# Kernel optimization log

Measured on AMD Instinct MI355X. Metric: run time of the kernel, lower is better.

Reference implementation:

```python
import jax, jax.numpy as jnp
import numpy as np

D, H, F, N, V, B, S, T = 512, 8, 2048, 2, 32000, 2, 1024, 1024


def _pe(seq_len, d):
    pos = np.arange(seq_len)[:, None].astype(np.float32)
    div = np.exp(np.arange(0, d, 2).astype(np.float32) * (-np.log(10000.0) / d))
    pe = np.zeros((seq_len, d), np.float32)
    pe[:, 0::2] = np.sin(pos * div)
    pe[:, 1::2] = np.cos(pos * div)
    return jnp.asarray(pe)


def _ln(x, g, b, eps=1e-6):
    # torch .var() default is unbiased (ddof=1)
    m = x.mean(-1, keepdims=True)
    v = jnp.sum((x - m) ** 2, -1, keepdims=True) / (x.shape[-1] - 1)
    return g * (x - m) / jnp.sqrt(v + eps) + b


def _mha(q, k, v, mask, w, b):
    # w: [4, D, D] (q,k,v,o); b: [4, D]
    Bq, Sq, Dm = q.shape
    Sk = k.shape[1]
    dk = Dm // H
    Q = (q @ w[0] + b[0]).reshape(Bq, Sq, H, dk).transpose(0, 2, 1, 3)
    K = (k @ w[1] + b[1]).reshape(Bq, Sk, H, dk).transpose(0, 2, 1, 3)
    Vv = (v @ w[2] + b[2]).reshape(Bq, Sk, H, dk).transpose(0, 2, 1, 3)
    s = jnp.einsum('bhqd,bhkd->bhqk', Q, K) / jnp.sqrt(jnp.float32(dk))
    s = jnp.where(mask == 0, jnp.float32(-1e9), s)
    a = jax.nn.softmax(s, axis=-1)
    o = jnp.einsum('bhqk,bhkd->bhqd', a, Vv).transpose(0, 2, 1, 3).reshape(Bq, Sq, Dm)
    return o @ w[3] + b[3]


def _ffn(x, w1, b1, w2, b2):
    return jax.nn.relu(x @ w1 + b1) @ w2 + b2


def _forward(src, tgt, src_mask, tgt_mask, p):
    (src_emb, tgt_emb, ea_w, ea_b, ef_w1, ef_b1, ef_w2, ef_b2, eln_g, eln_b, en_g, en_b,
     ds_w, ds_b, dc_w, dc_b, df_w1, df_b1, df_w2, df_b2, dln_g, dln_b, dn_g, dn_b, pw, pb) = p
    scale = jnp.sqrt(jnp.float32(D))
    # encoder
    x = src_emb[src] * scale + _pe(src.shape[1], D)
    for i in range(N):
        h = _ln(x, eln_g[i, 0], eln_b[i, 0])
        x = x + _mha(h, h, h, src_mask, ea_w[i], ea_b[i])
        h = _ln(x, eln_g[i, 1], eln_b[i, 1])
        x = x + _ffn(h, ef_w1[i], ef_b1[i], ef_w2[i], ef_b2[i])
    enc = _ln(x, en_g, en_b)
    # decoder
    y = tgt_emb[tgt] * scale + _pe(tgt.shape[1], D)
    for i in range(N):
        h = _ln(y, dln_g[i, 0], dln_b[i, 0])
        y = y + _mha(h, h, h, tgt_mask, ds_w[i], ds_b[i])
        h = _ln(y, dln_g[i, 1], dln_b[i, 1])
        y = y + _mha(h, enc, enc, src_mask, dc_w[i], dc_b[i])
        h = _ln(y, dln_g[i, 2], dln_b[i, 2])
        y = y + _ffn(h, df_w1[i], df_b1[i], df_w2[i], df_b2[i])
    y = _ln(y, dn_g, dn_b)
    return jax.nn.log_softmax(y @ pw + pb, axis=-1)


def setup_inputs() -> dict:
    key = jax.random.key(0)
    c = [0]
    def nk():
        c[0] += 1
        return jax.random.fold_in(key, c[0])
    def w(*s):
        return jax.random.normal(nk(), s, jnp.float32) * 0.02
    inp = {
        'src': jax.random.randint(nk(), (B, S), 0, V, jnp.int32),
        'tgt': jax.random.randint(nk(), (B, T), 0, V, jnp.int32),
        'src_mask': jnp.ones((B, 1, 1, S), jnp.int32),
        'tgt_mask': jnp.tril(jnp.ones((T, T), jnp.int32))[None, None],
        'src_emb': w(V, D), 'tgt_emb': w(V, D),
        'enc_attn_w': w(N, 4, D, D), 'enc_attn_b': jnp.zeros((N, 4, D), jnp.float32),
        'enc_ffn_w1': w(N, D, F), 'enc_ffn_b1': jnp.zeros((N, F), jnp.float32),
        'enc_ffn_w2': w(N, F, D), 'enc_ffn_b2': jnp.zeros((N, D), jnp.float32),
        'enc_ln_g': jnp.ones((N, 2, D), jnp.float32), 'enc_ln_b': jnp.zeros((N, 2, D), jnp.float32),
        'enc_norm_g': jnp.ones((D,), jnp.float32), 'enc_norm_b': jnp.zeros((D,), jnp.float32),
        'dec_self_w': w(N, 4, D, D), 'dec_self_b': jnp.zeros((N, 4, D), jnp.float32),
        'dec_cross_w': w(N, 4, D, D), 'dec_cross_b': jnp.zeros((N, 4, D), jnp.float32),
        'dec_ffn_w1': w(N, D, F), 'dec_ffn_b1': jnp.zeros((N, F), jnp.float32),
        'dec_ffn_w2': w(N, F, D), 'dec_ffn_b2': jnp.zeros((N, D), jnp.float32),
        'dec_ln_g': jnp.ones((N, 3, D), jnp.float32), 'dec_ln_b': jnp.zeros((N, 3, D), jnp.float32),
        'dec_norm_g': jnp.ones((D,), jnp.float32), 'dec_norm_b': jnp.zeros((D,), jnp.float32),
        'proj_w': w(D, V), 'proj_b': jnp.zeros((V,), jnp.float32),
    }
    return inp


def reference(src, tgt, src_mask, tgt_mask, src_emb, tgt_emb, enc_attn_w, enc_attn_b,
              enc_ffn_w1, enc_ffn_b1, enc_ffn_w2, enc_ffn_b2, enc_ln_g, enc_ln_b,
              enc_norm_g, enc_norm_b, dec_self_w, dec_self_b, dec_cross_w, dec_cross_b,
              dec_ffn_w1, dec_ffn_b1, dec_ffn_w2, dec_ffn_b2, dec_ln_g, dec_ln_b,
              dec_norm_g, dec_norm_b, proj_w, proj_b):
    p = (src_emb, tgt_emb, enc_attn_w, enc_attn_b, enc_ffn_w1, enc_ffn_b1, enc_ffn_w2,
         enc_ffn_b2, enc_ln_g, enc_ln_b, enc_norm_g, enc_norm_b, dec_self_w, dec_self_b,
         dec_cross_w, dec_cross_b, dec_ffn_w1, dec_ffn_b1, dec_ffn_w2, dec_ffn_b2,
         dec_ln_g, dec_ln_b, dec_norm_g, dec_norm_b, proj_w, proj_b)
    return _forward(src, tgt, src_mask, tgt_mask, p)
```

## Files before the change

### kernel.cpp

```cpp
#include <hip/hip_runtime.h>
#include <hip/hip_bf16.h>
#include <math.h>

using bf16 = __hip_bfloat16;
typedef float f32x4 __attribute__((ext_vector_type(4)));
typedef short short8 __attribute__((ext_vector_type(8)));

constexpr int kD = 512, kH = 8, kDk = 64, kF = 2048, kV = 32000;
constexpr int kB = 2, kS = 1024, kM = 2048, kBH = 16;

enum { ST_F32 = 0, ST_BF16, ST_QKV };

__device__ __forceinline__ void gload_lds16(const void* g, void* l) {
  __builtin_amdgcn_global_load_lds(
      (const __attribute__((address_space(1))) void*)g,
      (__attribute__((address_space(3))) void*)l, 16, 0, 0);
}

__device__ __forceinline__ float bfu2f(short u) {
  union { unsigned int i; float f; } c;
  c.i = ((unsigned int)(unsigned short)u) << 16;
  return c.f;
}

template <int BM, int BN, int STM, bool BIAS, bool RELU, bool RES, int NBUF, bool XSWZ,
          bool ASEL, bool DUAL>
__launch_bounds__(256)
__global__ void k_gemm(const bf16* __restrict__ A, int lda, long long Az,
                       const bf16* __restrict__ Bt, int ldb, long long Bz,
                       void* __restrict__ Cv, int ldc, long long Cz,
                       int K, float alpha,
                       const float* __restrict__ bias,
                       const float* __restrict__ res,
                       const bf16* __restrict__ A2,
                       const bf16* __restrict__ Bt2,
                       void* __restrict__ Cv2,
                       const float* __restrict__ bias2,
                       const float* __restrict__ res2) {
  constexpr int FM = BM / 32, FN = BN / 32;
  constexpr int LPS = BM / 32 + BN / 32;
  __shared__ __attribute__((aligned(16))) bf16 As[NBUF][BM * 64];
  __shared__ __attribute__((aligned(16))) bf16 Bs[NBUF][BN * 64];
  const int tid = threadIdx.x;
  const int w = tid >> 6, lane = tid & 63;
  int bx = blockIdx.x, by = blockIdx.y;
  if constexpr (DUAL) {
    const int half = gridDim.y >> 1;
    if (by >= half) {
      by -= half;
      A = A2; Bt = Bt2; Cv = Cv2; bias = bias2; res = res2;
    }
  }
  if constexpr (XSWZ) {
    const int nx = gridDim.x, ny = gridDim.y;
    const int lin = by * nx + bx;
    const int cpx = (nx * ny) >> 3;
    const int s = (lin & 7) * cpx + (lin >> 3);
    bx = s / ny;
    by = s - bx * ny;
  }
  const int bm = by * BM, bn = bx * BN;
  const int z = blockIdx.z;
  if constexpr (ASEL) { if (bn >= 512) A = A2; }
  A += (long long)z * Az;
  Bt += (long long)z * Bz;
  const int l15 = lane & 15, lhi = lane >> 4;
  const int wr = (w >> 1) * (BM / 2), wc = (w & 1) * (BN / 2);
  f32x4 acc[FM][FN] = {};
  const int nkt = K >> 6;

  auto stage = [&](int kt, int nb) {
#pragma unroll
    for (int it = 0; it < BM / 32; ++it) {
      int chunk = (it * 4 + w) * 64 + lane;
      int row = chunk >> 3, c = chunk & 7;
      int col = (c ^ (row & 7)) << 3;
      gload_lds16(A + (size_t)(bm + row) * lda + kt * 64 + col, As[nb] + (it * 4 + w) * 512);
    }
#pragma unroll
    for (int it = 0; it < BN / 32; ++it) {
      int chunk = (it * 4 + w) * 64 + lane;
      int row = chunk >> 3, c = chunk & 7;
      int col = (c ^ (row & 7)) << 3;
      gload_lds16(Bt + (size_t)(bn + row) * ldb + kt * 64 + col, Bs[nb] + (it * 4 + w) * 512);
    }
  };
  auto waitSteady = [&]() {
    if constexpr (LPS == 3) asm volatile("s_waitcnt vmcnt(6)" ::: "memory");
    else                    asm volatile("s_waitcnt vmcnt(8)" ::: "memory");
  };
  auto compute = [&](int cb) {
#pragma unroll
    for (int kk = 0; kk < 2; ++kk) {
      short8 af[FM], bf[FN];
#pragma unroll
      for (int i = 0; i < FM; ++i) {
        int row = wr + i * 16 + l15;
        af[i] = *(const short8*)(As[cb] + row * 64 + (((kk * 4 + lhi) ^ (row & 7)) * 8));
      }
#pragma unroll
      for (int j = 0; j < FN; ++j) {
        int row = wc + j * 16 + l15;
        bf[j] = *(const short8*)(Bs[cb] + row * 64 + (((kk * 4 + lhi) ^ (row & 7)) * 8));
      }
#pragma unroll
      for (int i = 0; i < FM; ++i)
#pragma unroll
        for (int j = 0; j < FN; ++j)
          acc[i][j] = __builtin_amdgcn_mfma_f32_16x16x32_bf16(af[i], bf[j], acc[i][j], 0, 0, 0);
    }
  };

  if constexpr (NBUF == 3) {
    stage(0, 0);
    stage(1, 1);
    stage(2, 2);
    waitSteady();
    __builtin_amdgcn_s_barrier();
    __builtin_amdgcn_sched_barrier(0);
    int cur = 0;
    for (int kt = 0; kt < nkt; ++kt) {
      compute(cur);
      asm volatile("s_waitcnt lgkmcnt(0)" ::: "memory");
      __builtin_amdgcn_sched_barrier(0);
      if (kt + 1 < nkt) {
        __builtin_amdgcn_s_barrier();
        if (kt + 3 < nkt) {
          stage(kt + 3, cur);
          waitSteady();
        } else {
          asm volatile("s_waitcnt vmcnt(0)" ::: "memory");
        }
        __builtin_amdgcn_s_barrier();
        __builtin_amdgcn_sched_barrier(0);
      }
      cur = (cur == 2) ? 0 : cur + 1;
    }
  } else {
    for (int kt = 0; kt < nkt; ++kt) {
      stage(kt, 0);
      __syncthreads();
      compute(0);
      __syncthreads();
    }
  }

#pragma unroll
  for (int i = 0; i < FM; ++i) {
#pragma unroll
    for (int j = 0; j < FN; ++j) {
#pragma unroll
      for (int r = 0; r < 4; ++r) {
        int m = bm + wr + i * 16 + lhi * 4 + r;
        int n = bn + wc + j * 16 + l15;
        float val = acc[i][j][r] * alpha;
        if constexpr (BIAS) val += bias[n];
        if constexpr (RELU) val = fmaxf(val, 0.f);
        if constexpr (RES) val += res[(size_t)m * ldc + n];
        if constexpr (STM == ST_F32) {
          ((float*)Cv)[(size_t)z * Cz + (size_t)m * ldc + n] = val;
        } else if constexpr (STM == ST_BF16) {
          ((bf16*)Cv)[(size_t)z * Cz + (size_t)m * ldc + n] = __float2bfloat16(val);
        } else if constexpr (STM == ST_QKV) {
          int seg = n >> 9, nn = n & 511;
          int b_ = m >> 10, s_ = m & 1023, h_ = nn >> 6, d_ = nn & 63;
          size_t idx = (seg < 2)
              ? (((size_t)(b_ * kH + h_) << 10) + s_) * kDk + d_
              : ((size_t)(b_ * kH + h_) * kDk + d_) * kS + s_;
          ((bf16*)Cv)[(size_t)seg * 1048576 + idx] = __float2bfloat16(val);
        }
      }
    }
  }
}

template <bool CAUSAL>
__launch_bounds__(256)
__global__ void k_fattn(const bf16* __restrict__ Q, const bf16* __restrict__ K,
                        const bf16* __restrict__ Vt, bf16* __restrict__ O) {
  __shared__ __attribute__((aligned(16))) bf16 Ks[3][4096];
  __shared__ __attribute__((aligned(16))) bf16 Vs[3][4096];
  __shared__ __attribute__((aligned(16))) bf16 Ps[4][1024];
  const int tid = threadIdx.x, w = tid >> 6, lane = tid & 63;
  const int l15 = lane & 15, lhi = lane >> 4;
  const int q0 = blockIdx.x * 64, bh = blockIdx.y;
  const int qw = q0 + w * 16;
  const bf16* Qp = Q + (((size_t)(bh << 10)) + qw + l15) * kDk;
  short8 aq[2];
  aq[0] = *(const short8*)(Qp + lhi * 8);
  aq[1] = *(const short8*)(Qp + 32 + lhi * 8);
  const int srow = w * 8 + (lane >> 3);
  const int sc = (lane & 7) ^ (srow & 7);
  const bf16* Ksrc = K + (((size_t)(bh << 10)) + srow) * kDk + sc * 8;
  const bf16* Vsrc = Vt + ((size_t)bh * kDk + srow) * kS + sc * 8;
  const int nt = CAUSAL ? (q0 >> 6) + 1 : (kS >> 6);

  auto stage = [&](int t, int nb) {
    int kv0 = t << 6;
    gload_lds16(Ksrc + (size_t)kv0 * kDk, Ks[nb] + w * 512);
    gload_lds16(Ksrc + (size_t)(kv0 + 32) * kDk, Ks[nb] + 2048 + w * 512);
    gload_lds16(Vsrc + kv0, Vs[nb] + w * 512);
    gload_lds16(Vsrc + kv0 + 32 * kS, Vs[nb] + 2048 + w * 512);
  };

  float m_[4], l_[4];
#pragma unroll
  for (int r = 0; r < 4; ++r) { m_[r] = -1e30f; l_[r] = 0.f; }
  f32x4 ao[4] = {};

  stage(0, 0);
  if (nt > 2) {
    stage(1, 1);
    stage(2, 2);
    asm volatile("s_waitcnt vmcnt(8)" ::: "memory");
  } else if (nt > 1) {
    stage(1, 1);
    asm volatile("s_waitcnt vmcnt(4)" ::: "memory");
  } else {
    asm volatile("s_waitcnt vmcnt(0)" ::: "memory");
  }
  __builtin_amdgcn_s_barrier();
  __builtin_amdgcn_sched_barrier(0);

  int cur = 0;
  for (int t = 0; t < nt; ++t) {
    f32x4 as[4] = {};
#pragma unroll
    for (int kk = 0; kk < 2; ++kk) {
      short8 bk[4];
#pragma unroll
      for (int nf = 0; nf < 4; ++nf) {
        int row = nf * 16 + l15;
        int c = (4 * kk + lhi) ^ (row & 7);
        bk[nf] = *(const short8*)(Ks[cur] + row * 64 + c * 8);
      }
#pragma unroll
      for (int nf = 0; nf < 4; ++nf)
        as[nf] = __builtin_amdgcn_mfma_f32_16x16x32_bf16(aq[kk], bk[nf], as[nf], 0, 0, 0);
    }
    float s[4][4];
#pragma unroll
    for (int nf = 0; nf < 4; ++nf)
#pragma unroll
      for (int r = 0; r < 4; ++r) {
        float v = as[nf][r] * 0.125f;
        if (CAUSAL && t == nt - 1) {
          int col = (t << 6) + nf * 16 + l15;
          int row = qw + lhi * 4 + r;
          if (col > row) v = -1e30f;
        }
        s[nf][r] = v;
      }
    float mn[4], scl[4], rsum[4];
#pragma unroll
    for (int r = 0; r < 4; ++r) {
      float mx = fmaxf(fmaxf(s[0][r], s[1][r]), fmaxf(s[2][r], s[3][r]));
      mx = fmaxf(mx, __shfl_xor(mx, 1));
      mx = fmaxf(mx, __shfl_xor(mx, 2));
      mx = fmaxf(mx, __shfl_xor(mx, 4));
      mx = fmaxf(mx, __shfl_xor(mx, 8));
      mn[r] = fmaxf(m_[r], mx);
      scl[r] = __expf(m_[r] - mn[r]);
      rsum[r] = 0.f;
    }
#pragma unroll
    for (int nf = 0; nf < 4; ++nf)
#pragma unroll
      for (int r = 0; r < 4; ++r) {
        float p = __expf(s[nf][r] - mn[r]);
        rsum[r] += p;
        int pr = lhi * 4 + r;
        int c = (2 * nf + (l15 >> 3)) ^ (pr & 7);
        Ps[w][pr * 64 + c * 8 + (l15 & 7)] = __float2bfloat16(p);
      }
#pragma unroll
    for (int r = 0; r < 4; ++r) {
      float su = rsum[r];
      su += __shfl_xor(su, 1);
      su += __shfl_xor(su, 2);
      su += __shfl_xor(su, 4);
      su += __shfl_xor(su, 8);
      l_[r] = l_[r] * scl[r] + su;
      m_[r] = mn[r];
    }
#pragma unroll
    for (int nf = 0; nf < 4; ++nf)
#pragma unroll
      for (int r = 0; r < 4; ++r) ao[nf][r] *= scl[r];
    asm volatile("s_waitcnt lgkmcnt(0)" ::: "memory");
    __builtin_amdgcn_sched_barrier(0);
#pragma unroll
    for (int kk = 0; kk < 2; ++kk) {
      short8 pa = *(const short8*)(Ps[w] + l15 * 64 + (((4 * kk + lhi) ^ (l15 & 7)) * 8));
      short8 bv[4];
#pragma unroll
      for (int nf = 0; nf < 4; ++nf) {
        int row = nf * 16 + l15;
        int c = (4 * kk + lhi) ^ (row & 7);
        bv[nf] = *(const short8*)(Vs[cur] + row * 64 + c * 8);
      }
#pragma unroll
      for (int nf = 0; nf < 4; ++nf)
        ao[nf] = __builtin_amdgcn_mfma_f32_16x16x32_bf16(pa, bv[nf], ao[nf], 0, 0, 0);
    }
    asm volatile("s_waitcnt lgkmcnt(0)" ::: "memory");
    __builtin_amdgcn_sched_barrier(0);
    if (t + 1 < nt) {
      __builtin_amdgcn_s_barrier();
      if (t + 3 < nt) {
        stage(t + 3, cur);
        asm volatile("s_waitcnt vmcnt(8)" ::: "memory");
      } else {
        asm volatile("s_waitcnt vmcnt(0)" ::: "memory");
      }
      __builtin_amdgcn_s_barrier();
      __builtin_amdgcn_sched_barrier(0);
    }
    cur = (cur == 2) ? 0 : cur + 1;
  }
  const int b_ = bh >> 3, h_ = bh & 7;
  float inv[4];
#pragma unroll
  for (int r = 0; r < 4; ++r) inv[r] = 1.f / l_[r];
#pragma unroll
  for (int nf = 0; nf < 4; ++nf)
#pragma unroll
    for (int r = 0; r < 4; ++r) {
      int q = qw + lhi * 4 + r;
      O[((size_t)(b_ * kS + q)) * kD + h_ * kDk + nf * 16 + l15] =
          __float2bfloat16(ao[nf][r] * inv[r]);
    }
}

struct TJobs {
  const float* src[8];
  bf16* dst[8];
  int K[8], N[8];
  int ofs[9];
};

struct PrepArgs {
  TJobs tj; int ntile;
  const int *src, *tgt;
  const float *src_emb, *tgt_emb;
  const float *eg, *eb, *dg, *db;
  float *x_enc, *x_dec;
  bf16 *hb_enc, *hb_dec;
};

__global__ void k_prep(PrepArgs P) {
  __shared__ float t[32][33];
  __shared__ float red[4], red2[4];
  const int tid = threadIdx.x;
  if ((int)blockIdx.x < P.ntile) {
    const int tb = blockIdx.x;
    int j = 0;
#pragma unroll
    for (int i = 1; i < 8; ++i) j += (tb >= P.tj.ofs[i]) ? 1 : 0;
    const int K = P.tj.K[j], N = P.tj.N[j];
    const int tn = N >> 5, tk = K >> 5;
    int r = tb - P.tj.ofs[j];
    const int z = r / (tn * tk);
    r -= z * tn * tk;
    const int k0 = (r / tn) << 5, n0 = (r % tn) << 5;
    const float* Wp = P.tj.src[j] + (size_t)z * K * N;
    bf16* WTp = P.tj.dst[j] + (size_t)z * K * N;
    const int tx = tid & 31, ty = tid >> 5;
#pragma unroll
    for (int rr = 0; rr < 32; rr += 8)
      t[ty + rr][tx] = Wp[(size_t)(k0 + ty + rr) * N + n0 + tx];
    __syncthreads();
#pragma unroll
    for (int rr = 0; rr < 32; rr += 8)
      WTp[(size_t)(n0 + ty + rr) * K + k0 + tx] = __float2bfloat16(t[tx][ty + rr]);
    return;
  }
  const int vb = blockIdx.x - P.ntile;
  const int m = vb & (kM - 1), which = vb >> 11;
  const int* tok = which ? P.tgt : P.src;
  const float* emb = which ? P.tgt_emb : P.src_emb;
  float* x = which ? P.x_dec : P.x_enc;
  const int s = m & (kS - 1);
  const float* e = emb + (size_t)tok[m] * kD;
  float* xp = x + (size_t)m * kD;
  float v[2];
#pragma unroll
  for (int h = 0; h < 2; ++h) {
    int d = tid + h * 256;
    int i = d >> 1;
    float freq = __expf(-(float)(2 * i) * (9.210340371976184f / 512.0f));
    float ang = (float)s * freq;
    float pe = (d & 1) ? cosf(ang) : sinf(ang);
    v[h] = e[d] * 22.62741699796952f + pe;
    xp[d] = v[h];
  }
  const int w = tid >> 6, lane = tid & 63;
  float sum = v[0] + v[1];
#pragma unroll
  for (int o = 32; o; o >>= 1) sum += __shfl_xor(sum, o);
  if (lane == 0) red[w] = sum;
  __syncthreads();
  sum = red[0] + red[1] + red[2] + red[3];
  const float mean = sum * (1.f / 512.f);
  float sq = (v[0] - mean) * (v[0] - mean) + (v[1] - mean) * (v[1] - mean);
#pragma unroll
  for (int o = 32; o; o >>= 1) sq += __shfl_xor(sq, o);
  if (lane == 0) red2[w] = sq;
  __syncthreads();
  sq = red2[0] + red2[1] + red2[2] + red2[3];
  const float rstd = rsqrtf(sq * (1.f / 511.f) + 1e-6f);
  const float* g = which ? P.dg : P.eg;
  const float* b = which ? P.db : P.eb;
  bf16* hb = (which ? P.hb_dec : P.hb_enc) + (size_t)m * kD;
#pragma unroll
  for (int h = 0; h < 2; ++h) {
    int d = tid + h * 256;
    hb[d] = __float2bfloat16(g[d] * (v[h] - mean) * rstd + b[d]);
  }
}

__global__ void k_ln(const float* __restrict__ x, const float* __restrict__ g,
                     const float* __restrict__ b, bf16* __restrict__ out) {
  int w = threadIdx.x >> 6, lane = threadIdx.x & 63;
  int row = blockIdx.x * 4 + w;
  const float* xp = x + (size_t)row * kD;
  float v[8];
  float sum = 0.f;
#pragma unroll
  for (int i = 0; i < 8; ++i) { v[i] = xp[lane + i * 64]; sum += v[i]; }
#pragma unroll
  for (int o = 32; o; o >>= 1) sum += __shfl_xor(sum, o);
  float mean = sum * (1.f / 512.f);
  float sq = 0.f;
#pragma unroll
  for (int i = 0; i < 8; ++i) { float d = v[i] - mean; sq += d * d; }
#pragma unroll
  for (int o = 32; o; o >>= 1) sq += __shfl_xor(sq, o);
  float inv = rsqrtf(sq * (1.f / 511.f) + 1e-6f);
  bf16* op = out + (size_t)row * kD;
#pragma unroll
  for (int i = 0; i < 8; ++i) {
    int d = lane + i * 64;
    op[d] = __float2bfloat16(g[d] * (v[i] - mean) * inv + b[d]);
  }
}

__global__ void k_ln2(const float* __restrict__ x1, const float* __restrict__ g1,
                      const float* __restrict__ b1, bf16* __restrict__ o1,
                      const float* __restrict__ x2, const float* __restrict__ g2,
                      const float* __restrict__ b2, bf16* __restrict__ o2) {
  const int which = blockIdx.y;
  const float* x = which ? x2 : x1;
  const float* g = which ? g2 : g1;
  const float* b = which ? b2 : b1;
  bf16* out = which ? o2 : o1;
  int w = threadIdx.x >> 6, lane = threadIdx.x & 63;
  int row = blockIdx.x * 4 + w;
  const float* xp = x + (size_t)row * kD;
  float v[8];
  float sum = 0.f;
#pragma unroll
  for (int i = 0; i < 8; ++i) { v[i] = xp[lane + i * 64]; sum += v[i]; }
#pragma unroll
  for (int o = 32; o; o >>= 1) sum += __shfl_xor(sum, o);
  float mean = sum * (1.f / 512.f);
  float sq = 0.f;
#pragma unroll
  for (int i = 0; i < 8; ++i) { float d = v[i] - mean; sq += d * d; }
#pragma unroll
  for (int o = 32; o; o >>= 1) sq += __shfl_xor(sq, o);
  float inv = rsqrtf(sq * (1.f / 511.f) + 1e-6f);
  bf16* op = out + (size_t)row * kD;
#pragma unroll
  for (int i = 0; i < 8; ++i) {
    int d = lane + i * 64;
    op[d] = __float2bfloat16(g[d] * (v[i] - mean) * inv + b[d]);
  }
}

__global__ __launch_bounds__(512, 1) void k_proj256(const bf16* __restrict__ A,
                                                    const bf16* __restrict__ Bt,
                                                    bf16* __restrict__ C,
                                                    const float* __restrict__ bias) {
  __shared__ __attribute__((aligned(16))) bf16 As[4][256 * 32];
  __shared__ __attribute__((aligned(16))) bf16 Bs[4][256 * 32];
  const int tid = threadIdx.x, w = tid >> 6, lane = tid & 63;
  const int l15 = lane & 15, lhi = lane >> 4;
  const int lin = blockIdx.y * 125 + blockIdx.x;
  const int s = (lin & 7) * 125 + (lin >> 3);
  const int bx = s >> 3, by = s & 7;
  const int bm = by * 256, bn = bx * 256;
  const int wr = (w >> 2) * 128, wc = (w & 3) * 64;
  const int rowq = tid >> 2, chk = tid & 3;
  const int swz = (chk ^ ((rowq >> 1) & 3)) << 3;
  const bf16* Asrc0 = A + (size_t)(bm + rowq) * kD + swz;
  const bf16* Asrc1 = A + (size_t)(bm + 128 + rowq) * kD + swz;
  const bf16* Bsrc0 = Bt + (size_t)(bn + rowq) * kD + swz;
  const bf16* Bsrc1 = Bt + (size_t)(bn + 128 + rowq) * kD + swz;
  const int ldsoff = w * 1024;

  auto stage = [&](int kt) {
    const int b = kt & 3;
    const int ko = kt * 32;
    gload_lds16(Asrc0 + ko, (char*)As[b] + ldsoff);
    gload_lds16(Asrc1 + ko, (char*)As[b] + 8192 + ldsoff);
    gload_lds16(Bsrc0 + ko, (char*)Bs[b] + ldsoff);
    gload_lds16(Bsrc1 + ko, (char*)Bs[b] + 8192 + ldsoff);
  };

  const int ra = wr + l15, rb = wc + l15;
  const int abase = ra * 64 + ((lhi ^ ((ra >> 1) & 3)) << 4);
  const int bbase = rb * 64 + ((lhi ^ ((rb >> 1) & 3)) << 4);

  f32x4 acc[8][4] = {};
  stage(0); stage(1); stage(2);
  for (int kt = 0; kt < 16; ++kt) {
    if (kt + 2 < 16)      asm volatile("s_waitcnt vmcnt(8)" ::: "memory");
    else if (kt + 1 < 16) asm volatile("s_waitcnt vmcnt(4)" ::: "memory");
    else                  asm volatile("s_waitcnt vmcnt(0)" ::: "memory");
    __builtin_amdgcn_s_barrier();
    __builtin_amdgcn_sched_barrier(0);
    if (kt + 3 < 16) stage(kt + 3);
    const int b = kt & 3;
    short8 af[8], bf[4];
#pragma unroll
    for (int i = 0; i < 8; ++i)
      af[i] = *(const short8*)((const char*)As[b] + abase + i * 1024);
#pragma unroll
    for (int j = 0; j < 4; ++j)
      bf[j] = *(const short8*)((const char*)Bs[b] + bbase + j * 1024);
#pragma unroll
    for (int i = 0; i < 8; ++i)
#pragma unroll
      for (int j = 0; j < 4; ++j)
        acc[i][j] = __builtin_amdgcn_mfma_f32_16x16x32_bf16(af[i], bf[j], acc[i][j], 0, 0, 0);
    asm volatile("s_waitcnt lgkmcnt(0)" ::: "memory");
    __builtin_amdgcn_sched_barrier(0);
  }
#pragma unroll
  for (int i = 0; i < 8; ++i)
#pragma unroll
    for (int j = 0; j < 4; ++j)
#pragma unroll
      for (int r = 0; r < 4; ++r) {
        int m = bm + wr + i * 16 + lhi * 4 + r;
        int n = bn + wc + j * 16 + l15;
        C[(size_t)m * kV + n] = __float2bfloat16(acc[i][j][r] + bias[n]);
      }
}

__global__ __launch_bounds__(640, 2) void k_lsm_bf(const bf16* __restrict__ L,
                                                   float* __restrict__ y) {
  const bf16* row = L + (size_t)blockIdx.x * kV;
  float* orow = y + (size_t)blockIdx.x * kV;
  const int t = threadIdx.x;
  const bool extra = t < 160;
  float v[56];
  float sum = 0.f;
#pragma unroll
  for (int i = 0; i < 6; ++i) {
    short8 s = *(const short8*)(row + (t + i * 640) * 8);
#pragma unroll
    for (int e = 0; e < 8; ++e) {
      float f = bfu2f(s[e]);
      v[i * 8 + e] = f;
      sum += __expf(f);
    }
  }
  if (extra) {
    short8 s = *(const short8*)(row + (3840 + t) * 8);
#pragma unroll
    for (int e = 0; e < 8; ++e) {
      float f = bfu2f(s[e]);
      v[48 + e] = f;
      sum += __expf(f);
    }
  }
#pragma unroll
  for (int o = 32; o; o >>= 1) sum += __shfl_xor(sum, o);
  __shared__ float red2[10];
  const int w = t >> 6, lane = t & 63;
  if (lane == 0) red2[w] = sum;
  __syncthreads();
  sum = 0.f;
#pragma unroll
  for (int i = 0; i < 10; ++i) sum += red2[i];
  const float sh = logf(sum);
#pragma unroll
  for (int i = 0; i < 6; ++i)
#pragma unroll
    for (int e = 0; e < 8; ++e) orow[(t + i * 640) * 8 + e] = v[i * 8 + e] - sh;
  if (extra)
#pragma unroll
    for (int e = 0; e < 8; ++e) orow[(3840 + t) * 8 + e] = v[48 + e] - sh;
}

extern "C" void kernel_launch(void* const* d_in, const int* in_sizes, int n_in,
                              void* d_out, int out_size, void* d_ws, size_t ws_size,
                              hipStream_t stream) {
  (void)in_sizes; (void)n_in; (void)out_size;
  if (ws_size < (size_t)212 * 1024 * 1024) return;

  const int* src = (const int*)d_in[0];
  const int* tgt = (const int*)d_in[1];
  const float* src_emb   = (const float*)d_in[4];
  const float* tgt_emb   = (const float*)d_in[5];
  const float* enc_attn_w = (const float*)d_in[6];
  const float* enc_attn_b = (const float*)d_in[7];
  const float* enc_ffn_w1 = (const float*)d_in[8];
  const float* enc_ffn_b1 = (const float*)d_in[9];
  const float* enc_ffn_w2 = (const float*)d_in[10];
  const float* enc_ffn_b2 = (const float*)d_in[11];
  const float* enc_ln_g  = (const float*)d_in[12];
  const float* enc_ln_b  = (const float*)d_in[13];
  const float* enc_norm_g = (const float*)d_in[14];
  const float* enc_norm_b = (const float*)d_in[15];
  const float* dec_self_w = (const float*)d_in[16];
  const float* dec_self_b = (const float*)d_in[17];
  const float* dec_cross_w = (const float*)d_in[18];
  const float* dec_cross_b = (const float*)d_in[19];
  const float* dec_ffn_w1 = (const float*)d_in[20];
  const float* dec_ffn_b1 = (const float*)d_in[21];
  const float* dec_ffn_w2 = (const float*)d_in[22];
  const float* dec_ffn_b2 = (const float*)d_in[23];
  const float* dec_ln_g  = (const float*)d_in[24];
  const float* dec_ln_b  = (const float*)d_in[25];
  const float* dec_norm_g = (const float*)d_in[26];
  const float* dec_norm_b = (const float*)d_in[27];
  const float* proj_w    = (const float*)d_in[28];
  const float* proj_b    = (const float*)d_in[29];

  char* ws = (char*)d_ws;
  auto MB = [](size_t x) { return x << 20; };
  bf16* enc_attn_wt  = (bf16*)(ws + MB(0));
  bf16* dec_self_wt  = (bf16*)(ws + MB(4));
  bf16* dec_cross_wt = (bf16*)(ws + MB(8));
  bf16* enc_f1t = (bf16*)(ws + MB(12));
  bf16* enc_f2t = (bf16*)(ws + MB(16));
  bf16* dec_f1t = (bf16*)(ws + MB(20));
  bf16* dec_f2t = (bf16*)(ws + MB(24));
  bf16* proj_wt = (bf16*)(ws + MB(28));
  float* x_enc  = (float*)(ws + MB(60));
  float* x_dec  = (float*)(ws + MB(64));
  bf16* hbuf    = (bf16*)(ws + MB(68));
  bf16* enc_bf  = (bf16*)(ws + MB(70));
  bf16* Qb      = (bf16*)(ws + MB(72));
  bf16* attn_o  = (bf16*)(ws + MB(78));
  bf16* logits  = (bf16*)(ws + MB(80));
  bf16* hbuf2   = (bf16*)(ws + MB(208));
  char* dob = (char*)d_out;
  bf16* ffn_mid = (bf16*)dob;
  bf16* Qb2     = (bf16*)(dob + MB(16));
  bf16* attn_o2 = (bf16*)(dob + MB(24));

  PrepArgs P;
  int acc = 0;
  auto setj = [&](int j, const float* s, bf16* d, int K, int N, int z) {
    P.tj.src[j] = s; P.tj.dst[j] = d; P.tj.K[j] = K; P.tj.N[j] = N; P.tj.ofs[j] = acc;
    acc += (K >> 5) * (N >> 5) * z;
  };
  setj(0, enc_attn_w, enc_attn_wt, 512, 512, 8);
  setj(1, dec_self_w, dec_self_wt, 512, 512, 8);
  setj(2, dec_cross_w, dec_cross_wt, 512, 512, 8);
  setj(3, enc_ffn_w1, enc_f1t, 512, 2048, 2);
  setj(4, enc_ffn_w2, enc_f2t, 2048, 512, 2);
  setj(5, dec_ffn_w1, dec_f1t, 512, 2048, 2);
  setj(6, dec_ffn_w2, dec_f2t, 2048, 512, 2);
  setj(7, proj_w, proj_wt, 512, 32000, 1);
  P.tj.ofs[8] = acc;
  P.ntile = acc;
  P.src = src; P.tgt = tgt;
  P.src_emb = src_emb; P.tgt_emb = tgt_emb;
  P.eg = enc_ln_g; P.eb = enc_ln_b;
  P.dg = dec_ln_g; P.db = dec_ln_b;
  P.x_enc = x_enc; P.x_dec = x_dec;
  P.hb_enc = hbuf; P.hb_dec = hbuf2;
  k_prep<<<acc + 2 * kM, 256, 0, stream>>>(P);

  auto qkv = [&](const bf16* aptr, const bf16* wt, const float* bias, const bf16* kvA) {
    if (kvA)
      k_gemm<64, 64, ST_QKV, true, false, false, 3, false, true, false>
          <<<dim3(24, 32, 1), 256, 0, stream>>>(
          aptr, 512, 0, wt, 512, 0, Qb, 0, 0, 512, 1.f, bias, nullptr, kvA,
          nullptr, nullptr, nullptr, nullptr);
    else
      k_gemm<64, 64, ST_QKV, true, false, false, 3, false, false, false>
          <<<dim3(24, 32, 1), 256, 0, stream>>>(
          aptr, 512, 0, wt, 512, 0, Qb, 0, 0, 512, 1.f, bias, nullptr, nullptr,
          nullptr, nullptr, nullptr, nullptr);
  };
  auto fattn = [&](bool causal, const bf16* qb, bf16* ao) {
    if (causal) k_fattn<true><<<dim3(16, kBH), 256, 0, stream>>>(qb, qb + 1048576, qb + 2097152, ao);
    else        k_fattn<false><<<dim3(16, kBH), 256, 0, stream>>>(qb, qb + 1048576, qb + 2097152, ao);
  };
  auto out_proj = [&](const bf16* ao, const bf16* wt, const float* bias, float* xio) {
    k_gemm<32, 64, ST_F32, true, false, true, 3, false, false, false>
        <<<dim3(8, 64, 1), 256, 0, stream>>>(
        ao, 512, 0, wt + 3 * 262144, 512, 0, xio, 512, 0, 512, 1.f, bias + 3 * 512,
        xio, nullptr, nullptr, nullptr, nullptr, nullptr);
  };
  auto LN = [&](const float* x, const float* g, const float* b, bf16* out) {
    k_ln<<<kM / 4, 256, 0, stream>>>(x, g, b, out);
  };
  auto ffn = [&](float* xio, const bf16* w1t, const float* b1, const bf16* w2t,
                 const float* b2) {
    k_gemm<64, 64, ST_BF16, true, true, false, 3, false, false, false>
        <<<dim3(32, 32, 1), 256, 0, stream>>>(
        hbuf, 512, 0, w1t, 512, 0, ffn_mid, kF, 0, 512, 1.f, b1, nullptr, nullptr,
        nullptr, nullptr, nullptr, nullptr);
    k_gemm<32, 64, ST_F32, true, false, true, 3, false, false, false>
        <<<dim3(8, 64, 1), 256, 0, stream>>>(
        ffn_mid, 2048, 0, w2t, 2048, 0, xio, 512, 0, 2048, 1.f, b2, xio, nullptr,
        nullptr, nullptr, nullptr, nullptr);
  };

  k_gemm<64, 64, ST_QKV, true, false, false, 3, false, false, true>
      <<<dim3(24, 64, 1), 256, 0, stream>>>(
      hbuf, 512, 0, enc_attn_wt, 512, 0, Qb, 0, 0, 512, 1.f, enc_attn_b, nullptr,
      hbuf2, dec_self_wt, Qb2, dec_self_b, nullptr);
  fattn(false, Qb, attn_o);
  fattn(true, Qb2, attn_o2);
  k_gemm<32, 64, ST_F32, true, false, true, 3, false, false, true>
      <<<dim3(8, 128, 1), 256, 0, stream>>>(
      attn_o, 512, 0, enc_attn_wt + 3 * 262144, 512, 0, x_enc, 512, 0, 512, 1.f,
      enc_attn_b + 3 * 512, x_enc,
      attn_o2, dec_self_wt + 3 * 262144, x_dec, dec_self_b + 3 * 512, x_dec);
  k_ln2<<<dim3(kM / 4, 2), 256, 0, stream>>>(
      x_enc, enc_ln_g + 512, enc_ln_b + 512, hbuf,
      x_dec, dec_ln_g + 512, dec_ln_b + 512, hbuf2);

  ffn(x_enc, enc_f1t, enc_ffn_b1, enc_f2t, enc_ffn_b2);
  LN(x_enc, enc_ln_g + 1024, enc_ln_b + 1024, hbuf);
  qkv(hbuf, enc_attn_wt + 1048576, enc_attn_b + 2048, nullptr);
  fattn(false, Qb, attn_o);
  out_proj(attn_o, enc_attn_wt + 1048576, enc_attn_b + 2048, x_enc);
  LN(x_enc, enc_ln_g + 1024 + 512, enc_ln_b + 1024 + 512, hbuf);
  ffn(x_enc, enc_f1t + 1048576, enc_ffn_b1 + 2048, enc_f2t + 1048576, enc_ffn_b2 + 512);
  LN(x_enc, enc_norm_g, enc_norm_b, enc_bf);

  for (int i = 0; i < 2; ++i) {
    const bf16* wts = dec_self_wt + (size_t)i * 1048576;
    const float* bs = dec_self_b + i * 2048;
    const bf16* wtc = dec_cross_wt + (size_t)i * 1048576;
    const float* bc = dec_cross_b + i * 2048;
    if (i == 1) {
      LN(x_dec, dec_ln_g + 1536, dec_ln_b + 1536, hbuf);
      qkv(hbuf, wts, bs, nullptr);
      fattn(true, Qb, attn_o);
      out_proj(attn_o, wts, bs, x_dec);
      LN(x_dec, dec_ln_g + 1536 + 512, dec_ln_b + 1536 + 512, hbuf);
    }
    const bf16* qsrc = (i == 0) ? hbuf2 : hbuf;
    qkv(qsrc, wtc, bc, enc_bf);
    fattn(false, Qb, attn_o);
    out_proj(attn_o, wtc, bc, x_dec);
    LN(x_dec, dec_ln_g + i * 1536 + 1024, dec_ln_b + i * 1536 + 1024, hbuf);
    ffn(x_dec, dec_f1t + (size_t)i * 1048576, dec_ffn_b1 + i * 2048,
        dec_f2t + (size_t)i * 1048576, dec_ffn_b2 + i * 512);
  }
  LN(x_dec, dec_norm_g, dec_norm_b, hbuf);

  k_proj256<<<dim3(125, 8), 512, 0, stream>>>(hbuf, proj_wt, logits, proj_b);
  k_lsm_bf<<<kM, 640, 0, stream>>>(logits, (float*)d_out);
}
```

Measured before the change: 662.4 us.

## Merge encoder and causal decoder attention into one launch; raise MFMA wave priority

Pulls the flash-attention body into a device function and adds a combined kernel. That kernel runs the encoder non-causal attention and the decoder causal self-attention in one grid, picking the job from blockIdx.y. This removes one launch and lets the short causal blocks fill the gaps left by the longer ones. It also wraps the MFMA sections of the attention and projection GEMM loops in s_setprio to favour the waves that are issuing matrix work. Causal is now a runtime flag, which may add branches or registers inside the inner loop.

```diff
diff --git a/kernel.cpp b/kernel.cpp
--- a/kernel.cpp
+++ b/kernel.cpp
@@ -174,16 +174,15 @@
   }
 }
 
-template <bool CAUSAL>
-__launch_bounds__(256)
-__global__ void k_fattn(const bf16* __restrict__ Q, const bf16* __restrict__ K,
-                        const bf16* __restrict__ Vt, bf16* __restrict__ O) {
-  __shared__ __attribute__((aligned(16))) bf16 Ks[3][4096];
-  __shared__ __attribute__((aligned(16))) bf16 Vs[3][4096];
-  __shared__ __attribute__((aligned(16))) bf16 Ps[4][1024];
+__device__ __forceinline__ void fattn_body(const bf16* __restrict__ Q,
+                                           const bf16* __restrict__ K,
+                                           const bf16* __restrict__ Vt,
+                                           bf16* __restrict__ O,
+                                           int q0, int bh, bool causal,
+                                           bf16 (*Ks)[4096], bf16 (*Vs)[4096],
+                                           bf16 (*Ps)[1024]) {
   const int tid = threadIdx.x, w = tid >> 6, lane = tid & 63;
   const int l15 = lane & 15, lhi = lane >> 4;
-  const int q0 = blockIdx.x * 64, bh = blockIdx.y;
   const int qw = q0 + w * 16;
   const bf16* Qp = Q + (((size_t)(bh << 10)) + qw + l15) * kDk;
   short8 aq[2];
@@ -193,7 +192,7 @@
   const int sc = (lane & 7) ^ (srow & 7);
   const bf16* Ksrc = K + (((size_t)(bh << 10)) + srow) * kDk + sc * 8;
   const bf16* Vsrc = Vt + ((size_t)bh * kDk + srow) * kS + sc * 8;
-  const int nt = CAUSAL ? (q0 >> 6) + 1 : (kS >> 6);
+  const int nt = causal ? (q0 >> 6) + 1 : (kS >> 6);
 
   auto stage = [&](int t, int nb) {
     int kv0 = t << 6;
@@ -225,6 +224,7 @@
   int cur = 0;
   for (int t = 0; t < nt; ++t) {
     f32x4 as[4] = {};
+    __builtin_amdgcn_s_setprio(1);
 #pragma unroll
     for (int kk = 0; kk < 2; ++kk) {
       short8 bk[4];
@@ -238,13 +238,14 @@
       for (int nf = 0; nf < 4; ++nf)
         as[nf] = __builtin_amdgcn_mfma_f32_16x16x32_bf16(aq[kk], bk[nf], as[nf], 0, 0, 0);
     }
+    __builtin_amdgcn_s_setprio(0);
     float s[4][4];
 #pragma unroll
     for (int nf = 0; nf < 4; ++nf)
 #pragma unroll
       for (int r = 0; r < 4; ++r) {
         float v = as[nf][r] * 0.125f;
-        if (CAUSAL && t == nt - 1) {
+        if (causal && t == nt - 1) {
           int col = (t << 6) + nf * 16 + l15;
           int row = qw + lhi * 4 + r;
           if (col > row) v = -1e30f;
@@ -289,6 +290,7 @@
       for (int r = 0; r < 4; ++r) ao[nf][r] *= scl[r];
     asm volatile("s_waitcnt lgkmcnt(0)" ::: "memory");
     __builtin_amdgcn_sched_barrier(0);
+    __builtin_amdgcn_s_setprio(1);
 #pragma unroll
     for (int kk = 0; kk < 2; ++kk) {
       short8 pa = *(const short8*)(Ps[w] + l15 * 64 + (((4 * kk + lhi) ^ (l15 & 7)) * 8));
@@ -303,6 +305,7 @@
       for (int nf = 0; nf < 4; ++nf)
         ao[nf] = __builtin_amdgcn_mfma_f32_16x16x32_bf16(pa, bv[nf], ao[nf], 0, 0, 0);
     }
+    __builtin_amdgcn_s_setprio(0);
     asm volatile("s_waitcnt lgkmcnt(0)" ::: "memory");
     __builtin_amdgcn_sched_barrier(0);
     if (t + 1 < nt) {
@@ -330,6 +333,28 @@
       O[((size_t)(b_ * kS + q)) * kD + h_ * kDk + nf * 16 + l15] =
           __float2bfloat16(ao[nf][r] * inv[r]);
     }
+}
+
+template <bool CAUSAL>
+__launch_bounds__(256)
+__global__ void k_fattn(const bf16* __restrict__ Q, const bf16* __restrict__ K,
+                        const bf16* __restrict__ Vt, bf16* __restrict__ O) {
+  __shared__ __attribute__((aligned(16))) bf16 Ks[3][4096];
+  __shared__ __attribute__((aligned(16))) bf16 Vs[3][4096];
+  __shared__ __attribute__((aligned(16))) bf16 Ps[4][1024];
+  fattn_body(Q, K, Vt, O, blockIdx.x * 64, blockIdx.y, CAUSAL, Ks, Vs, Ps);
+}
+
+__launch_bounds__(256)
+__global__ void k_fattn2(const bf16* __restrict__ Q1, bf16* __restrict__ O1, int c1,
+                         const bf16* __restrict__ Q2, bf16* __restrict__ O2, int c2) {
+  __shared__ __attribute__((aligned(16))) bf16 Ks[3][4096];
+  __shared__ __attribute__((aligned(16))) bf16 Vs[3][4096];
+  __shared__ __attribute__((aligned(16))) bf16 Ps[4][1024];
+  int by = blockIdx.y;
+  const bf16* Q = Q1; bf16* O = O1; bool causal = c1;
+  if (by >= kBH) { by -= kBH; Q = Q2; O = O2; causal = c2; }
+  fattn_body(Q, Q + 1048576, Q + 2097152, O, blockIdx.x * 64, by, causal, Ks, Vs, Ps);
 }
 
 struct TJobs {
@@ -529,11 +554,13 @@
 #pragma unroll
     for (int j = 0; j < 4; ++j)
       bf[j] = *(const short8*)((const char*)Bs[b] + bbase + j * 1024);
+    __builtin_amdgcn_s_setprio(1);
 #pragma unroll
     for (int i = 0; i < 8; ++i)
 #pragma unroll
       for (int j = 0; j < 4; ++j)
         acc[i][j] = __builtin_amdgcn_mfma_f32_16x16x32_bf16(af[i], bf[j], acc[i][j], 0, 0, 0);
+    __builtin_amdgcn_s_setprio(0);
     asm volatile("s_waitcnt lgkmcnt(0)" ::: "memory");
     __builtin_amdgcn_sched_barrier(0);
   }
@@ -718,8 +745,7 @@
       <<<dim3(24, 64, 1), 256, 0, stream>>>(
       hbuf, 512, 0, enc_attn_wt, 512, 0, Qb, 0, 0, 512, 1.f, enc_attn_b, nullptr,
       hbuf2, dec_self_wt, Qb2, dec_self_b, nullptr);
-  fattn(false, Qb, attn_o);
-  fattn(true, Qb2, attn_o2);
+  k_fattn2<<<dim3(16, 2 * kBH), 256, 0, stream>>>(Qb, attn_o, 0, Qb2, attn_o2, 1);
   k_gemm<32, 64, ST_F32, true, false, true, 3, false, false, true>
       <<<dim3(8, 128, 1), 256, 0, stream>>>(
       attn_o, 512, 0, enc_attn_wt + 3 * 262144, 512, 0, x_enc, 512, 0, 512, 1.f,
```

Result: faster. 645.2 us (-2.6%).
